# Kernel optimization log

Measured on AMD Instinct MI355X. Metric: run time of the kernel, lower is better.

Reference implementation:

```python
import jax, jax.numpy as jnp
import numpy as np

# Fixed rendering constants (non-tensor forward args of the module)
THETA_RANGE = (0.0, float(np.pi) / 2.0)
PHI_RANGE = (-float(np.pi) / 2.0, float(np.pi) / 2.0)
R_RANGE = (0.5, 2.5)
C_LIGHT = 1.0          # speed of light (normalized units)
DELTA_T = 0.03125      # time-bin width -> step = C_LIGHT*DELTA_T = (2.0/64)
SCALING_MODIFIER = 1.0
USE_OCCLUSION = True
SH_C0 = 0.28209479177387814
G = 2048


def quat_to_rotmat(q):
    # q: [G,4] (w,x,y,z), unnormalized -> [G,3,3]
    q = q / (jnp.linalg.norm(q, axis=-1, keepdims=True) + 1e-12)
    w, x, y, z = q[:, 0], q[:, 1], q[:, 2], q[:, 3]
    R = jnp.stack([
        1 - 2 * (y * y + z * z), 2 * (x * y - w * z), 2 * (x * z + w * y),
        2 * (x * y + w * z), 1 - 2 * (x * x + z * z), 2 * (y * z - w * x),
        2 * (x * z - w * y), 2 * (y * z + w * x), 1 - 2 * (x * x + y * y),
    ], axis=-1)
    return R.reshape(-1, 3, 3)


def setup_inputs() -> dict:
    key = jax.random.key(0)
    k1, k2, k3, k4, k5 = jax.random.split(key, 5)
    # Gaussians clustered in front of the sensor (camera at origin, +z hemisphere)
    gaussian_means = jax.random.normal(k1, (G, 3), jnp.float32) * 0.5 + jnp.array([0.0, 0.0, 1.5], jnp.float32)
    gaussian_scales = jax.random.normal(k2, (G, 3), jnp.float32) * 0.3 - 2.5   # log-scales -> exp ~ 0.08
    gaussian_rotations = jax.random.normal(k3, (G, 4), jnp.float32)
    gaussian_opacities = jax.random.normal(k4, (G, 1), jnp.float32)
    gaussian_features = jax.random.normal(k5, (G, 3), jnp.float32) * 0.5
    camera_pos = jnp.zeros((3,), jnp.float32)
    return {
        "gaussian_means": gaussian_means,
        "gaussian_scales": gaussian_scales,
        "gaussian_rotations": gaussian_rotations,
        "gaussian_opacities": gaussian_opacities,
        "gaussian_features": gaussian_features,
        "camera_pos": camera_pos,
        "num_theta": 32,
        "num_phi": 32,
        "num_r": 64,
    }


def reference(gaussian_means, gaussian_scales, gaussian_rotations,
              gaussian_opacities, gaussian_features, camera_pos,
              num_theta, num_phi, num_r):
    # --- ray construction (module wrapper) ---
    theta = jnp.linspace(THETA_RANGE[0], THETA_RANGE[1], num_theta)
    phi = jnp.linspace(PHI_RANGE[0], PHI_RANGE[1], num_phi)
    tg, pg = jnp.meshgrid(theta, phi, indexing='ij')           # [nt,np]
    th, ph = tg.reshape(-1), pg.reshape(-1)                    # [R]
    dirs = jnp.stack([jnp.sin(th) * jnp.cos(ph),
                      jnp.sin(th) * jnp.sin(ph),
                      jnp.cos(th)], axis=1)                    # [R,3]
    t = jnp.linspace(R_RANGE[0], R_RANGE[1], num_r)            # [S]

    # --- Gaussian parameter activation ---
    scales = jnp.exp(gaussian_scales) * SCALING_MODIFIER       # [G,3]
    Rm = quat_to_rotmat(gaussian_rotations)                    # [G,3,3]
    inv_s2 = 1.0 / (scales * scales)                           # [G,3]
    prec = jnp.einsum('gij,gj,gkj->gik', Rm, inv_s2, Rm)       # Sigma^{-1} [G,3,3]
    opac = jax.nn.sigmoid(gaussian_opacities[:, 0])            # [G]
    albedo = jnp.mean(jnp.clip(SH_C0 * gaussian_features + 0.5, 0.0, None), axis=-1)  # [G]

    # --- per-(sample,ray,gaussian) Mahalanobis quadratic, factored in t ---
    # (o + t d - mu)^T P (o + t d - mu) = A[r,g] t^2 + B[r,g] t + Cq[g]
    om = camera_pos[None, :] - gaussian_means                  # [G,3]
    A = jnp.einsum('rd,gde,re->rg', dirs, prec, dirs)          # [R,G]
    B = 2.0 * jnp.einsum('rd,gde,ge->rg', dirs, prec, om)      # [R,G]
    Cq = jnp.einsum('gd,gde,ge->g', om, prec, om)              # [G]
    t2 = t * t
    quad = (A[None] * t2[:, None, None]
            + B[None] * t[:, None, None]
            + Cq[None, None])                                  # [S,R,G]
    w = opac[None, None, :] * jnp.exp(-0.5 * quad)             # [S,R,G]
    density = jnp.sum(w, axis=-1)                              # [S,R]
    rho = jnp.sum(w * albedo[None, None, :], axis=-1)          # [S,R]

    # --- sequential transmittance accumulation along the ray ---
    step = C_LIGHT * DELTA_T
    acc = jnp.cumsum(density * step, axis=0)
    acc_excl = jnp.concatenate([jnp.zeros_like(acc[:1]), acc[:-1]], axis=0)
    transmittance = jnp.exp(-acc_excl)                         # [S,R]
    rho_density = rho * transmittance if USE_OCCLUSION else rho

    # --- module post-processing ---
    result = rho_density.reshape(num_r, num_theta, num_phi)
    result = result / (t[:, None, None] ** 2 + 1e-8) * jnp.sin(tg)[None]
    dtheta = (THETA_RANGE[1] - THETA_RANGE[0]) / num_theta
    dphi = (PHI_RANGE[1] - PHI_RANGE[0]) / num_phi
    pred_histogram = jnp.sum(result, axis=(1, 2)) * dtheta * dphi
    return result, pred_histogram
```

## Files before the change

### kernel.cpp

```cpp
#include <hip/hip_runtime.h>
#include <math.h>

#define G_N   2048
#define NT    32
#define NP    32
#define NR    64
#define NRAY  (NT * NP)
#define PLANE 8196

__global__ __launch_bounds__(512, 4) void k_main(
    const float* __restrict__ means, const float* __restrict__ scales,
    const float* __restrict__ rots, const float* __restrict__ opacs,
    const float* __restrict__ feats, const float* __restrict__ cam,
    float* __restrict__ out) {
  __shared__ float coef[2 * PLANE];
  __shared__ float red[2][8][128];

  const int tid  = threadIdx.x;
  const int ray0 = blockIdx.x * 2;
  const int ti   = ray0 >> 5;
  const int pj0  = ray0 & 31;

  const float dth = (float)(M_PI / 2.0 / (NT - 1));
  const float dph = (float)(M_PI / (NP - 1));
  float sth, cth;
  sincosf((float)ti * dth, &sth, &cth);
  const float dz = cth, dzz = dz * dz;

  float dX[2], dY[2], dXX[2], dYY[2], dXY[2], dXZ[2], dYZ[2];
  #pragma unroll
  for (int r = 0; r < 2; ++r) {
    float ph = (float)(-M_PI / 2.0) + (float)(pj0 + r) * dph;
    float sp, cp;
    sincosf(ph, &sp, &cp);
    float dx = sth * cp, dy = sth * sp;
    dX[r] = dx; dY[r] = dy;
    dXX[r] = dx * dx; dYY[r] = dy * dy;
    dXY[r] = 2.f * dx * dy; dXZ[r] = 2.f * dx * dz; dYZ[r] = 2.f * dy * dz;
  }

  const float cx = cam[0], cy = cam[1], cz = cam[2];
  const float c      = -0.7213475204444817f;
  const float l2e    = 1.4426950408889634f;
  const float n2l2e  = -2.8853900817779268f;
  const float SH_C0  = 0.28209479177387814f;

  #pragma unroll
  for (int i = 0; i < G_N / 512; ++i) {
    int g = tid + i * 512;
    float i0 = __builtin_amdgcn_exp2f(n2l2e * scales[3*g+0]);
    float i1 = __builtin_amdgcn_exp2f(n2l2e * scales[3*g+1]);
    float i2 = __builtin_amdgcn_exp2f(n2l2e * scales[3*g+2]);

    float qw = rots[4*g+0], qx = rots[4*g+1], qy = rots[4*g+2], qz = rots[4*g+3];
    float inv = __builtin_amdgcn_rsqf(qw*qw + qx*qx + qy*qy + qz*qz);
    qw *= inv; qx *= inv; qy *= inv; qz *= inv;

    float R00 = 1.f - 2.f*(qy*qy + qz*qz), R01 = 2.f*(qx*qy - qw*qz), R02 = 2.f*(qx*qz + qw*qy);
    float R10 = 2.f*(qx*qy + qw*qz), R11 = 1.f - 2.f*(qx*qx + qz*qz), R12 = 2.f*(qy*qz - qw*qx);
    float R20 = 2.f*(qx*qz - qw*qy), R21 = 2.f*(qy*qz + qw*qx), R22 = 1.f - 2.f*(qx*qx + qy*qy);

    float p00 = c*(R00*R00*i0 + R01*R01*i1 + R02*R02*i2);
    float p11 = c*(R10*R10*i0 + R11*R11*i1 + R12*R12*i2);
    float p22 = c*(R20*R20*i0 + R21*R21*i1 + R22*R22*i2);
    float p01 = c*(R00*R10*i0 + R01*R11*i1 + R02*R12*i2);
    float p02 = c*(R00*R20*i0 + R01*R21*i1 + R02*R22*i2);
    float p12 = c*(R10*R20*i0 + R11*R21*i1 + R12*R22*i2);

    float ox = cx - means[3*g+0], oy = cy - means[3*g+1], oz = cz - means[3*g+2];
    float Px = p00*ox + p01*oy + p02*oz;
    float Py = p01*ox + p11*oy + p12*oz;
    float Pz = p02*ox + p12*oy + p22*oz;
    float Cq = ox*Px + oy*Py + oz*Pz;

    float u = __builtin_amdgcn_exp2f(-l2e * opacs[g]);
    float Cf = Cq - __builtin_amdgcn_logf(1.0f + u);

    float a0 = fmaxf(SH_C0*feats[3*g+0] + 0.5f, 0.f);
    float a1 = fmaxf(SH_C0*feats[3*g+1] + 0.5f, 0.f);
    float a2 = fmaxf(SH_C0*feats[3*g+2] + 0.5f, 0.f);
    float alb = (a0 + a1 + a2) * (1.0f/3.0f);

    #pragma unroll
    for (int r = 0; r < 2; ++r) {
      float A = p00*dXX[r] + p11*dYY[r] + p22*dzz + p01*dXY[r] + p02*dXZ[r] + p12*dYZ[r];
      float B = 2.f * (Px*dX[r] + Py*dY[r] + Pz*dz);
      *(float4*)&coef[r * PLANE + g * 4] = make_float4(A, B, Cf, alb);
    }
  }
  __syncthreads();

  const int lane = tid & 63;
  const int wv   = tid >> 6;
  const int r    = lane >> 5;
  const int ts   = lane & 31;
  const float tstep = 2.0f / 63.0f;
  const float t0 = 0.5f + (float)ts * tstep;
  const float t1 = t0 + 32.f * tstep;

  const float4* basep = (const float4*)&coef[r * PLANE] + wv * (G_N / 8);
  float d0 = 0.f, d1 = 0.f;
  float h0 = 0.f, h1 = 0.f;
  #pragma unroll 8
  for (int g = 0; g < G_N / 8; ++g) {
    float4 e = basep[g];
    float q0 = fmaf(fmaf(e.x, t0, e.y), t0, e.z);
    float q1 = fmaf(fmaf(e.x, t1, e.y), t1, e.z);
    float x0 = __builtin_amdgcn_exp2f(q0);
    float x1 = __builtin_amdgcn_exp2f(q1);
    d0 += x0; h0 = fmaf(x0, e.w, h0);
    d1 += x1; h1 = fmaf(x1, e.w, h1);
  }

  red[0][wv][r*64 + ts     ] = d0;  red[1][wv][r*64 + ts     ] = h0;
  red[0][wv][r*64 + ts + 32] = d1;  red[1][wv][r*64 + ts + 32] = h1;
  __syncthreads();

  if (tid < 128) {
    const int rr = tid >> 6;
    const int t  = tid & 63;
    int idx = rr * 64 + t;
    float D  = ((red[0][0][idx] + red[0][1][idx]) + (red[0][2][idx] + red[0][3][idx]))
             + ((red[0][4][idx] + red[0][5][idx]) + (red[0][6][idx] + red[0][7][idx]));
    float Rh = ((red[1][0][idx] + red[1][1][idx]) + (red[1][2][idx] + red[1][3][idx]))
             + ((red[1][4][idx] + red[1][5][idx]) + (red[1][6][idx] + red[1][7][idx]));
    const float step = 1.0f * 0.03125f;
    float s = D * step;
    float inc = s;
    #pragma unroll
    for (int off = 1; off < 64; off <<= 1) {
      float v = __shfl_up(inc, off, 64);
      if (t >= off) inc += v;
    }
    float excl = inc - s;
    float T = __builtin_amdgcn_exp2f(-1.4426950408889634f * excl);
    float tv = 0.5f + (float)t * tstep;
    float res = Rh * T / (tv * tv + 1e-8f) * sth;
    out[t * NRAY + ray0 + rr] = res;
  }
}

__global__ __launch_bounds__(256) void k_hist(const float* __restrict__ res,
                                              float* __restrict__ hist) {
  const int t = blockIdx.x;
  const int tid = threadIdx.x;
  float s = 0.f;
  #pragma unroll
  for (int rr = tid; rr < NRAY; rr += 256) s += res[t * NRAY + rr];
  #pragma unroll
  for (int off = 32; off > 0; off >>= 1) s += __shfl_down(s, off, 64);
  __shared__ float sm[4];
  if ((tid & 63) == 0) sm[tid >> 6] = s;
  __syncthreads();
  if (tid == 0) {
    const float dtdp = (float)((M_PI / 2.0 / NT) * (M_PI / NP));
    hist[t] = ((sm[0] + sm[1]) + (sm[2] + sm[3])) * dtdp;
  }
}

extern "C" void kernel_launch(void* const* d_in, const int* in_sizes, int n_in,
                              void* d_out, int out_size, void* d_ws, size_t ws_size,
                              hipStream_t stream) {
  const float* means  = (const float*)d_in[0];
  const float* scales = (const float*)d_in[1];
  const float* rots   = (const float*)d_in[2];
  const float* opacs  = (const float*)d_in[3];
  const float* feats  = (const float*)d_in[4];
  const float* cam    = (const float*)d_in[5];

  float* out = (float*)d_out;

  k_main<<<NRAY / 2, 512, 0, stream>>>(means, scales, rots, opacs, feats, cam, out);
  k_hist<<<NR,       256, 0, stream>>>(out, out + NR * NRAY);
}
```

Measured before the change: 94.43 us.

## Split coefficient precompute into separate kernel writing per-ray coefficients to workspace

Moves the per-Gaussian quadratic coefficient computation into a separate kernel that writes one float4 per ray and Gaussian to global workspace. The main kernel then streams these from global memory with one ray per 256-thread block instead of staging two rays in LDS. This aims to shrink LDS use and raise occupancy in the exp-heavy loop. In exchange it adds a large global write/read round trip and an extra kernel launch, while the precompute is still redone per ray.

```diff
diff --git a/kernel.cpp b/kernel.cpp
--- a/kernel.cpp
+++ b/kernel.cpp
@@ -6,38 +6,24 @@
 #define NP    32
 #define NR    64
 #define NRAY  (NT * NP)
-#define PLANE 8196
 
-__global__ __launch_bounds__(512, 4) void k_main(
+__global__ __launch_bounds__(256) void k_pre(
     const float* __restrict__ means, const float* __restrict__ scales,
     const float* __restrict__ rots, const float* __restrict__ opacs,
     const float* __restrict__ feats, const float* __restrict__ cam,
-    float* __restrict__ out) {
-  __shared__ float coef[2 * PLANE];
-  __shared__ float red[2][8][128];
-
-  const int tid  = threadIdx.x;
-  const int ray0 = blockIdx.x * 2;
-  const int ti   = ray0 >> 5;
-  const int pj0  = ray0 & 31;
+    float4* __restrict__ cf) {
+  const int ray = blockIdx.x;
+  const int ti  = ray >> 5;
+  const int pj  = ray & 31;
 
   const float dth = (float)(M_PI / 2.0 / (NT - 1));
   const float dph = (float)(M_PI / (NP - 1));
-  float sth, cth;
+  float sth, cth, sp, cp;
   sincosf((float)ti * dth, &sth, &cth);
-  const float dz = cth, dzz = dz * dz;
-
-  float dX[2], dY[2], dXX[2], dYY[2], dXY[2], dXZ[2], dYZ[2];
-  #pragma unroll
-  for (int r = 0; r < 2; ++r) {
-    float ph = (float)(-M_PI / 2.0) + (float)(pj0 + r) * dph;
-    float sp, cp;
-    sincosf(ph, &sp, &cp);
-    float dx = sth * cp, dy = sth * sp;
-    dX[r] = dx; dY[r] = dy;
-    dXX[r] = dx * dx; dYY[r] = dy * dy;
-    dXY[r] = 2.f * dx * dy; dXZ[r] = 2.f * dx * dz; dYZ[r] = 2.f * dy * dz;
-  }
+  sincosf((float)(-M_PI / 2.0) + (float)pj * dph, &sp, &cp);
+  const float dx = sth * cp, dy = sth * sp, dz = cth;
+  const float dxx = dx*dx, dyy = dy*dy, dzz = dz*dz;
+  const float dxy = 2.f*dx*dy, dxz = 2.f*dx*dz, dyz = 2.f*dy*dz;
 
   const float cx = cam[0], cy = cam[1], cz = cam[2];
   const float c      = -0.7213475204444817f;
@@ -45,9 +31,10 @@
   const float n2l2e  = -2.8853900817779268f;
   const float SH_C0  = 0.28209479177387814f;
 
+  const int tid = threadIdx.x;
   #pragma unroll
-  for (int i = 0; i < G_N / 512; ++i) {
-    int g = tid + i * 512;
+  for (int i = 0; i < G_N / 256; ++i) {
+    int g = tid + i * 256;
     float i0 = __builtin_amdgcn_exp2f(n2l2e * scales[3*g+0]);
     float i1 = __builtin_amdgcn_exp2f(n2l2e * scales[3*g+1]);
     float i2 = __builtin_amdgcn_exp2f(n2l2e * scales[3*g+2]);
@@ -62,7 +49,8 @@
 
     float p00 = c*(R00*R00*i0 + R01*R01*i1 + R02*R02*i2);
     float p11 = c*(R10*R10*i0 + R11*R11*i1 + R12*R12*i2);
-    float p22 = c*(R20*R20*i0 + R21*R21*i1 + R22*R22*i2);
+    float p22 = c*(R20*R20*i0 + R21*R21*i1 + R02*0.f + R22*R22*i2);
+    p22 = c*(R20*R20*i0 + R21*R21*i1 + R22*R22*i2);
     float p01 = c*(R00*R10*i0 + R01*R11*i1 + R02*R12*i2);
     float p02 = c*(R00*R20*i0 + R01*R21*i1 + R02*R22*i2);
     float p12 = c*(R10*R20*i0 + R11*R21*i1 + R12*R22*i2);
@@ -73,7 +61,7 @@
     float Pz = p02*ox + p12*oy + p22*oz;
     float Cq = ox*Px + oy*Py + oz*Pz;
 
-    float u = __builtin_amdgcn_exp2f(-l2e * opacs[g]);
+    float u  = __builtin_amdgcn_exp2f(-l2e * opacs[g]);
     float Cf = Cq - __builtin_amdgcn_logf(1.0f + u);
 
     float a0 = fmaxf(SH_C0*feats[3*g+0] + 0.5f, 0.f);
@@ -81,62 +69,58 @@
     float a2 = fmaxf(SH_C0*feats[3*g+2] + 0.5f, 0.f);
     float alb = (a0 + a1 + a2) * (1.0f/3.0f);
 
-    #pragma unroll
-    for (int r = 0; r < 2; ++r) {
-      float A = p00*dXX[r] + p11*dYY[r] + p22*dzz + p01*dXY[r] + p02*dXZ[r] + p12*dYZ[r];
-      float B = 2.f * (Px*dX[r] + Py*dY[r] + Pz*dz);
-      *(float4*)&coef[r * PLANE + g * 4] = make_float4(A, B, Cf, alb);
-    }
+    float A = p00*dxx + p11*dyy + p22*dzz + p01*dxy + p02*dxz + p12*dyz;
+    float B = 2.f * (Px*dx + Py*dy + Pz*dz);
+
+    cf[(size_t)ray * G_N + g] = make_float4(A, B, Cf, alb);
   }
+}
+
+__global__ __launch_bounds__(256, 4) void k_main(
+    const float4* __restrict__ cf, float* __restrict__ out) {
+  __shared__ float red[2][4][64];
+
+  const int tid  = threadIdx.x;
+  const int ray  = blockIdx.x;
+  const int wv   = tid >> 6;
+  const int lane = tid & 63;
+
+  const float tstep = 2.0f / 63.0f;
+  const float t  = 0.5f + (float)lane * tstep;
+  const float t2 = t * t;
+
+  const float4* __restrict__ p = cf + (size_t)ray * G_N + wv * (G_N / 4);
+  float d = 0.f, h = 0.f;
+  #pragma unroll 8
+  for (int g = 0; g < G_N / 4; ++g) {
+    float4 e = p[g];
+    float q = fmaf(e.y, t, e.x * t2) + e.z;
+    float x = __builtin_amdgcn_exp2f(q);
+    d += x;
+    h = fmaf(x, e.w, h);
+  }
+  red[0][wv][lane] = d;
+  red[1][wv][lane] = h;
   __syncthreads();
 
-  const int lane = tid & 63;
-  const int wv   = tid >> 6;
-  const int r    = lane >> 5;
-  const int ts   = lane & 31;
-  const float tstep = 2.0f / 63.0f;
-  const float t0 = 0.5f + (float)ts * tstep;
-  const float t1 = t0 + 32.f * tstep;
-
-  const float4* basep = (const float4*)&coef[r * PLANE] + wv * (G_N / 8);
-  float d0 = 0.f, d1 = 0.f;
-  float h0 = 0.f, h1 = 0.f;
-  #pragma unroll 8
-  for (int g = 0; g < G_N / 8; ++g) {
-    float4 e = basep[g];
-    float q0 = fmaf(fmaf(e.x, t0, e.y), t0, e.z);
-    float q1 = fmaf(fmaf(e.x, t1, e.y), t1, e.z);
-    float x0 = __builtin_amdgcn_exp2f(q0);
-    float x1 = __builtin_amdgcn_exp2f(q1);
-    d0 += x0; h0 = fmaf(x0, e.w, h0);
-    d1 += x1; h1 = fmaf(x1, e.w, h1);
-  }
-
-  red[0][wv][r*64 + ts     ] = d0;  red[1][wv][r*64 + ts     ] = h0;
-  red[0][wv][r*64 + ts + 32] = d1;  red[1][wv][r*64 + ts + 32] = h1;
-  __syncthreads();
-
-  if (tid < 128) {
-    const int rr = tid >> 6;
-    const int t  = tid & 63;
-    int idx = rr * 64 + t;
-    float D  = ((red[0][0][idx] + red[0][1][idx]) + (red[0][2][idx] + red[0][3][idx]))
-             + ((red[0][4][idx] + red[0][5][idx]) + (red[0][6][idx] + red[0][7][idx]));
-    float Rh = ((red[1][0][idx] + red[1][1][idx]) + (red[1][2][idx] + red[1][3][idx]))
-             + ((red[1][4][idx] + red[1][5][idx]) + (red[1][6][idx] + red[1][7][idx]));
+  if (tid < 64) {
+    float D  = (red[0][0][tid] + red[0][1][tid]) + (red[0][2][tid] + red[0][3][tid]);
+    float Rh = (red[1][0][tid] + red[1][1][tid]) + (red[1][2][tid] + red[1][3][tid]);
     const float step = 1.0f * 0.03125f;
     float s = D * step;
     float inc = s;
     #pragma unroll
     for (int off = 1; off < 64; off <<= 1) {
       float v = __shfl_up(inc, off, 64);
-      if (t >= off) inc += v;
+      if (tid >= off) inc += v;
     }
     float excl = inc - s;
     float T = __builtin_amdgcn_exp2f(-1.4426950408889634f * excl);
-    float tv = 0.5f + (float)t * tstep;
+    float tv = 0.5f + (float)tid * tstep;
+    const float dth = (float)(M_PI / 2.0 / (NT - 1));
+    float sth = sinf((float)(ray >> 5) * dth);
     float res = Rh * T / (tv * tv + 1e-8f) * sth;
-    out[t * NRAY + ray0 + rr] = res;
+    out[tid * NRAY + ray] = res;
   }
 }
 
@@ -168,8 +152,10 @@
   const float* feats  = (const float*)d_in[4];
   const float* cam    = (const float*)d_in[5];
 
-  float* out = (float*)d_out;
+  float4* cf  = (float4*)d_ws;
+  float*  out = (float*)d_out;
 
-  k_main<<<NRAY / 2, 512, 0, stream>>>(means, scales, rots, opacs, feats, cam, out);
-  k_hist<<<NR,       256, 0, stream>>>(out, out + NR * NRAY);
+  k_pre <<<NRAY, 256, 0, stream>>>(means, scales, rots, opacs, feats, cam, cf);
+  k_main<<<NRAY, 256, 0, stream>>>(cf, out);
+  k_hist<<<NR,   256, 0, stream>>>(out, out + NR * NRAY);
 }
```

New measurement: 157.6 us. +66.9%, slower.
